# Optimization experiments

Measured on AMD Instinct MI355X. Metric: run time of the kernel, lower is better.

The kernel has to match this reference:

```python
import jax, jax.numpy as jnp
import numpy as np

COST_CLASS, COST_BBOX, COST_GIOU = 1.0, 5.0, 2.0
BS, Q, K, T = 16, 1024, 256, 128


def setup_inputs() -> dict:
    key = jax.random.key(0)
    k1, k2, k3, k4 = jax.random.split(key, 4)
    pred_logits = jax.random.normal(k1, (BS, Q, K), dtype=jnp.float32)
    # predicted boxes in (mid, width) format, width > 0
    pred_boxes = jax.random.uniform(k2, (BS, Q, 2), dtype=jnp.float32, minval=0.05, maxval=1.0)
    # target boxes in (x0, x1) format with x0 < x1
    tgt_boxes = jnp.sort(jax.random.uniform(k3, (BS, T, 2), dtype=jnp.float32), axis=-1)
    tgt_labels = jax.random.randint(k4, (BS, T), 0, K, dtype=jnp.int32)
    return {"pred_logits": pred_logits, "pred_boxes": pred_boxes,
            "tgt_boxes": tgt_boxes, "tgt_labels": tgt_labels}


def midwtoxy(x):
    mid, w = x[..., 0], x[..., 1]
    return jnp.stack([mid - 0.5 * w, mid + 0.5 * w], axis=-1)


def getgiou(b1, b2):
    # b1: [N,2] (x0,x1), b2: [M,2]; returns [N,M] generalized IoU for 1-D intervals
    area1 = b1[:, 1] - b1[:, 0]              # [N]
    area2 = b2[:, 1] - b2[:, 0]              # [M]
    lt = jnp.maximum(b1[:, None, 0], b2[None, :, 0])
    rb = jnp.minimum(b1[:, None, 1], b2[None, :, 1])
    inter = jnp.clip(rb - lt, 0.0)           # [N,M]
    union = area1[:, None] + area2[None, :] - inter
    iou = inter / union
    hull_lt = jnp.minimum(b1[:, None, 0], b2[None, :, 0])
    hull_rb = jnp.maximum(b1[:, None, 1], b2[None, :, 1])
    hull = jnp.clip(hull_rb - hull_lt, 0.0)
    return iou - (hull - union) / hull


def reference(pred_logits, pred_boxes, tgt_boxes, tgt_labels):
    bs, q, k = pred_logits.shape
    out_prob = jax.nn.softmax(pred_logits.reshape(bs * q, k), axis=-1)  # [bs*Q, K]
    out_bbox = midwtoxy(pred_boxes.reshape(bs * q, 2))                  # [bs*Q, 2] (x0,x1)
    tgt_bbox = tgt_boxes.reshape(-1, 2)                                 # [bs*T, 2]
    tgt_ids = tgt_labels.reshape(-1)                                    # [bs*T]

    cost_class = -out_prob[:, tgt_ids]                                  # [bs*Q, bs*T]
    # L1 cdist over 2 coords, without materializing a [N,M,2] tensor
    cost_bbox = (jnp.abs(out_bbox[:, None, 0] - tgt_bbox[None, :, 0]) +
                 jnp.abs(out_bbox[:, None, 1] - tgt_bbox[None, :, 1]))
    cost_giou = -getgiou(out_bbox, tgt_bbox)

    C = COST_BBOX * cost_bbox + COST_CLASS * cost_class + COST_GIOU * cost_giou
    # [bs, Q, bs*T]; the original feeds the per-sample diagonal blocks
    # C[b, :, b*T:(b+1)*T] to scipy linear_sum_assignment (CPU, non-differentiable,
    # excluded from this GPU-math baseline).
    return C.reshape(bs, q, -1)
```

## Files before the change

### kernel.cpp

```cpp
#include <hip/hip_runtime.h>

#define BS 16
#define Q  1024
#define K  256
#define T  128
#define NROWS (BS * Q)
#define M     (BS * T)
#define RPB   8

__device__ __forceinline__ float cost_fn(float x0, float x1, float w1,
                                         float tx0, float tx1, float w2,
                                         float p) {
    float l1   = fabsf(x0 - tx0) + fabsf(x1 - tx1);
    float ir   = fminf(x1, tx1) - fmaxf(x0, tx0);
    float s    = w1 + w2;
    float inter= fmaxf(ir, 0.0f);
    float mn   = fminf(ir, 0.0f);
    float uni  = s - inter;
    float hull = s - ir;
    float giou = (inter * hull + mn * uni) * __builtin_amdgcn_rcpf(uni * hull);
    return fmaf(5.0f, l1, -p) - 2.0f * giou;
}

__global__ __launch_bounds__(256) void hungarian_cost_kernel(
    const float* __restrict__ pred_logits,
    const float* __restrict__ pred_boxes,
    const float* __restrict__ tgt_boxes,
    const int*   __restrict__ tgt_labels,
    float* __restrict__ out)
{
    __shared__ float probs[RPB][K];
    __shared__ float rbox[RPB][3];

    const int t    = threadIdx.x;
    const int w    = t >> 6;
    const int lane = t & 63;
    const int row0 = blockIdx.x * RPB;

    #pragma unroll
    for (int r = 0; r < 2; ++r) {
        int lr = 2 * w + r;
        int n  = row0 + lr;
        float4 v = ((const float4*)(pred_logits + (size_t)n * K))[lane];
        float e0 = __expf(v.x), e1 = __expf(v.y), e2 = __expf(v.z), e3 = __expf(v.w);
        float sum = (e0 + e1) + (e2 + e3);
        #pragma unroll
        for (int off = 1; off < 64; off <<= 1)
            sum += __shfl_xor(sum, off, 64);
        float rs = __builtin_amdgcn_rcpf(sum);
        float4 pv; pv.x = e0 * rs; pv.y = e1 * rs; pv.z = e2 * rs; pv.w = e3 * rs;
        ((float4*)&probs[lr][0])[lane] = pv;
        if (lane == 0) {
            float mid = pred_boxes[(size_t)n * 2 + 0];
            float ww  = pred_boxes[(size_t)n * 2 + 1];
            rbox[lr][0] = mid - 0.5f * ww;
            rbox[lr][1] = mid + 0.5f * ww;
            rbox[lr][2] = ww;
        }
    }
    __syncthreads();

    float rx0[RPB], rx1[RPB], rw1[RPB];
    #pragma unroll
    for (int r = 0; r < RPB; ++r) {
        rx0[r] = rbox[r][0]; rx1[r] = rbox[r][1]; rw1[r] = rbox[r][2];
    }

    const float4* tb4 = (const float4*)tgt_boxes;
    const int4*   tl4 = (const int4*)tgt_labels;

    #pragma unroll
    for (int c = 0; c < 2; ++c) {
        int vv = t + c * 256;
        float4 b01 = tb4[2 * vv];
        float4 b23 = tb4[2 * vv + 1];
        int4   lab = tl4[vv];

        float w2a = b01.y - b01.x;
        float w2b = b01.w - b01.z;
        float w2c = b23.y - b23.x;
        float w2d = b23.w - b23.z;

        #pragma unroll
        for (int r = 0; r < RPB; ++r) {
            float x0 = rx0[r], x1 = rx1[r], w1 = rw1[r];
            const float* prow = &probs[r][0];
            float4 rr;
            rr.x = cost_fn(x0, x1, w1, b01.x, b01.y, w2a, prow[lab.x]);
            rr.y = cost_fn(x0, x1, w1, b01.z, b01.w, w2b, prow[lab.y]);
            rr.z = cost_fn(x0, x1, w1, b23.x, b23.y, w2c, prow[lab.z]);
            rr.w = cost_fn(x0, x1, w1, b23.z, b23.w, w2d, prow[lab.w]);
            ((float4*)(out + (size_t)(row0 + r) * M))[vv] = rr;
        }
    }
}

extern "C" void kernel_launch(void* const* d_in, const int* in_sizes, int n_in,
                              void* d_out, int out_size, void* d_ws, size_t ws_size,
                              hipStream_t stream) {
    const float* pred_logits = (const float*)d_in[0];
    const float* pred_boxes  = (const float*)d_in[1];
    const float* tgt_boxes   = (const float*)d_in[2];
    const int*   tgt_labels  = (const int*)d_in[3];
    float* out = (float*)d_out;

    hungarian_cost_kernel<<<NROWS / RPB, 256, 0, stream>>>(
        pred_logits, pred_boxes, tgt_boxes, tgt_labels, out);
}
```

Measured before the change: 151.5 us.

## Transpose softmax probs in LDS and double rows per block

Each block now handles 16 prediction rows instead of 8, halving the grid and the number of times target boxes and labels are reloaded per row. Softmax probabilities are transposed in shared memory into a label-major layout padded to 20, so one 128-bit LDS read fetches a label's probability for four rows instead of one scalar gathered read per row. Row boxes are loaded once into a vector array, and launch bounds request 4 blocks per CU. In exchange the kernel needs an extra transpose pass and barrier, more shared memory, and more register pressure.

```diff
diff --git a/kernel.cpp b/kernel.cpp
--- a/kernel.cpp
+++ b/kernel.cpp
@@ -6,7 +6,10 @@
 #define T  128
 #define NROWS (BS * Q)
 #define M     (BS * T)
-#define RPB   8
+#define RPB   16
+#define PTS   20
+
+typedef float v4f __attribute__((ext_vector_type(4)));
 
 __device__ __forceinline__ float cost_fn(float x0, float x1, float w1,
                                          float tx0, float tx1, float w2,
@@ -22,7 +25,7 @@
     return fmaf(5.0f, l1, -p) - 2.0f * giou;
 }
 
-__global__ __launch_bounds__(256) void hungarian_cost_kernel(
+__global__ __launch_bounds__(256, 4) void hungarian_cost_kernel(
     const float* __restrict__ pred_logits,
     const float* __restrict__ pred_boxes,
     const float* __restrict__ tgt_boxes,
@@ -30,18 +33,28 @@
     float* __restrict__ out)
 {
     __shared__ float probs[RPB][K];
-    __shared__ float rbox[RPB][3];
+    __shared__ float probsT[K][PTS];
+    __shared__ v4f   rbox4[RPB];
 
     const int t    = threadIdx.x;
     const int w    = t >> 6;
     const int lane = t & 63;
     const int row0 = blockIdx.x * RPB;
 
+    if (t < RPB) {
+        float2 mw = ((const float2*)pred_boxes)[row0 + t];
+        v4f rb;
+        rb.x = mw.x - 0.5f * mw.y;
+        rb.y = mw.x + 0.5f * mw.y;
+        rb.z = mw.y;
+        rb.w = 0.0f;
+        rbox4[t] = rb;
+    }
+
     #pragma unroll
-    for (int r = 0; r < 2; ++r) {
-        int lr = 2 * w + r;
-        int n  = row0 + lr;
-        float4 v = ((const float4*)(pred_logits + (size_t)n * K))[lane];
+    for (int r = 0; r < 4; ++r) {
+        int lr = 4 * w + r;
+        float4 v = ((const float4*)(pred_logits + (size_t)(row0 + lr) * K))[lane];
         float e0 = __expf(v.x), e1 = __expf(v.y), e2 = __expf(v.z), e3 = __expf(v.w);
         float sum = (e0 + e1) + (e2 + e3);
         #pragma unroll
@@ -50,47 +63,54 @@
         float rs = __builtin_amdgcn_rcpf(sum);
         float4 pv; pv.x = e0 * rs; pv.y = e1 * rs; pv.z = e2 * rs; pv.w = e3 * rs;
         ((float4*)&probs[lr][0])[lane] = pv;
-        if (lane == 0) {
-            float mid = pred_boxes[(size_t)n * 2 + 0];
-            float ww  = pred_boxes[(size_t)n * 2 + 1];
-            rbox[lr][0] = mid - 0.5f * ww;
-            rbox[lr][1] = mid + 0.5f * ww;
-            rbox[lr][2] = ww;
+    }
+    __syncthreads();
+
+    {
+        float c[RPB];
+        #pragma unroll
+        for (int lr = 0; lr < RPB; ++lr)
+            c[lr] = probs[lr][t];
+        #pragma unroll
+        for (int c4 = 0; c4 < 4; ++c4) {
+            v4f pv; pv.x = c[4*c4]; pv.y = c[4*c4+1]; pv.z = c[4*c4+2]; pv.w = c[4*c4+3];
+            *(v4f*)&probsT[t][4 * c4] = pv;
         }
     }
     __syncthreads();
-
-    float rx0[RPB], rx1[RPB], rw1[RPB];
-    #pragma unroll
-    for (int r = 0; r < RPB; ++r) {
-        rx0[r] = rbox[r][0]; rx1[r] = rbox[r][1]; rw1[r] = rbox[r][2];
-    }
 
     const float4* tb4 = (const float4*)tgt_boxes;
     const int4*   tl4 = (const int4*)tgt_labels;
 
     #pragma unroll
-    for (int c = 0; c < 2; ++c) {
-        int vv = t + c * 256;
+    for (int g = 0; g < 2; ++g) {
+        const int vv = t + g * 256;
         float4 b01 = tb4[2 * vv];
         float4 b23 = tb4[2 * vv + 1];
         int4   lab = tl4[vv];
-
         float w2a = b01.y - b01.x;
         float w2b = b01.w - b01.z;
         float w2c = b23.y - b23.x;
         float w2d = b23.w - b23.z;
+        float* obase = out + (size_t)row0 * M + 4 * vv;
 
         #pragma unroll
-        for (int r = 0; r < RPB; ++r) {
-            float x0 = rx0[r], x1 = rx1[r], w1 = rw1[r];
-            const float* prow = &probs[r][0];
-            float4 rr;
-            rr.x = cost_fn(x0, x1, w1, b01.x, b01.y, w2a, prow[lab.x]);
-            rr.y = cost_fn(x0, x1, w1, b01.z, b01.w, w2b, prow[lab.y]);
-            rr.z = cost_fn(x0, x1, w1, b23.x, b23.y, w2c, prow[lab.z]);
-            rr.w = cost_fn(x0, x1, w1, b23.z, b23.w, w2d, prow[lab.w]);
-            ((float4*)(out + (size_t)(row0 + r) * M))[vv] = rr;
+        for (int c = 0; c < 4; ++c) {
+            const int lr0 = 4 * c;
+            v4f pa = *(const v4f*)&probsT[lab.x][lr0];
+            v4f pb = *(const v4f*)&probsT[lab.y][lr0];
+            v4f pc = *(const v4f*)&probsT[lab.z][lr0];
+            v4f pd = *(const v4f*)&probsT[lab.w][lr0];
+            #pragma unroll
+            for (int r = 0; r < 4; ++r) {
+                v4f rb = rbox4[lr0 + r];
+                float4 rr;
+                rr.x = cost_fn(rb.x, rb.y, rb.z, b01.x, b01.y, w2a, pa[r]);
+                rr.y = cost_fn(rb.x, rb.y, rb.z, b01.z, b01.w, w2b, pb[r]);
+                rr.z = cost_fn(rb.x, rb.y, rb.z, b23.x, b23.y, w2c, pc[r]);
+                rr.w = cost_fn(rb.x, rb.y, rb.z, b23.z, b23.w, w2d, pd[r]);
+                *(float4*)(obase + (size_t)(lr0 + r) * M) = rr;
+            }
         }
     }
 }
```

Measured after the change: 150.4 us. No clear change (-0.7%).
